# Performance work log

Hardware: AMD Instinct MI355X
Metric: run time of the kernel (lower is better)

The kernel has to match this reference:

```python
import jax, jax.numpy as jnp
import numpy as np
from jax import lax

# Static model/config sizes
B, ANG, C, H, NF, NB = 1, 9, 3, 128, 16, 2


def get_freq_position(n):
    """Anti-diagonal frequency bands of an n x n angular-DCT grid (python/static)."""
    bands = []
    for i in range(n):
        bands.append(([i], [0]))
    for j in range(1, n):
        bands.append(([n - 1], [j]))
    for item in bands:
        while item[0][0] > 0 and item[1][0] < n - 1:
            item[0].insert(0, item[0][0] - 1)
            item[1].insert(0, item[1][0] + 1)
    return bands


def dct_mat(n):
    """Orthonormal DCT-II matrix (row k = k-th basis)."""
    k = jnp.arange(n, dtype=jnp.float32)[:, None]
    i = jnp.arange(n, dtype=jnp.float32)[None, :]
    m = jnp.cos(jnp.pi * (i + 0.5) * k / n) * jnp.sqrt(2.0 / n)
    return m.at[0].multiply(1.0 / np.sqrt(2.0))


def conv3d(x, w, b):
    # x: (N, Cin, D, H, W), w: (Cout, Cin, 3, 3, 3)
    y = lax.conv_general_dilated(x, w, (1, 1, 1), 'SAME',
                                 dimension_numbers=('NCDHW', 'OIDHW', 'NCDHW'))
    return y + b[None, :, None, None, None]


def branch(cut, wi, bi, a, wb, bb):
    """init conv + NB ResBlock3D (PReLU -> Conv3d, residual), plus outer skip."""
    y0 = conv3d(cut, wi, bi)
    y = y0
    for k in range(NB):
        r = jnp.where(y >= 0, y, a[k] * y)  # PReLU (single-parameter)
        y = y + conv3d(r, wb[k], bb[k])
    return y0 + y


def setup_inputs() -> dict:
    key = jax.random.key(0)
    ks = jax.random.split(key, 32)

    def nrm(k, shape, s=0.05):
        return jax.random.normal(k, shape, dtype=jnp.float32) * s

    inp = {"x": jax.random.normal(ks[0], (B, ANG, ANG, C, H, H), dtype=jnp.float32)}
    i = 1
    for n in ("dc", "lo", "mi", "hi"):
        inp[f"w_{n}_i"] = nrm(ks[i], (NF, C, 3, 3, 3)); i += 1
        inp[f"b_{n}_i"] = nrm(ks[i], (NF,)); i += 1
        inp[f"a_{n}"] = jnp.full((NB,), 0.25, dtype=jnp.float32)
        inp[f"w_{n}"] = nrm(ks[i], (NB, NF, NF, 3, 3, 3)); i += 1
        inp[f"b_{n}"] = nrm(ks[i], (NB, NF)); i += 1
    inp["w_last"] = nrm(ks[i], (C, NF))  # 1x1 Conv2d, no bias
    return inp


def reference(x, w_dc_i, b_dc_i, a_dc, w_dc, b_dc,
              w_lo_i, b_lo_i, a_lo, w_lo, b_lo,
              w_mi_i, b_mi_i, a_mi, w_mi, b_mi,
              w_hi_i, b_hi_i, a_hi, w_hi, b_hi, w_last):
    b, u, v, c, h, w = x.shape
    Da = dct_mat(u)  # angular DCT (u == v)
    Ds = dct_mat(h)  # spatial DCT (h == w)

    # SpaAngDCT: spatial 2D DCT then angular 2D DCT
    xf = jnp.einsum('buvchw,Hh,Ww->buvcHW', x, Ds, Ds)
    xf = jnp.einsum('buvchw,Uu,Vv->bUVchw', xf, Da, Da)

    x_rec = jnp.zeros((b, NF, u, v, h, w), dtype=x.dtype)
    for idx, (ui, vi) in enumerate(get_freq_position(u)):
        if idx == 0:
            p = (w_dc_i, b_dc_i, a_dc, w_dc, b_dc)
        elif idx <= 2:
            p = (w_lo_i, b_lo_i, a_lo, w_lo, b_lo)
        elif idx <= u - 1:
            p = (w_mi_i, b_mi_i, a_mi, w_mi, b_mi)
        else:
            p = (w_hi_i, b_hi_i, a_hi, w_hi, b_hi)
        ua, va = jnp.array(ui), jnp.array(vi)
        cut = xf[:, ua, va].transpose(0, 2, 1, 3, 4)  # (b, c, L, h, w)
        out = branch(cut, *p)                          # (b, NF, L, h, w)
        x_rec = x_rec.at[:, :, ua, va].set(out)        # scatter band back

    # 'b c u v h w -> b c (u h) (v w)' then 1x1 conv (NF -> 3)
    xr = x_rec.transpose(0, 1, 2, 4, 3, 5).reshape(b, NF, u * h, v * w)
    xr = jnp.einsum('bnHW,on->boHW', xr, w_last)
    xr = xr.reshape(b, c, u, h, v, w).transpose(0, 2, 4, 1, 3, 5)  # (b,u,v,c,h,w)

    # InverseSpaAngDCT: angular IDCT then spatial IDCT
    xr = jnp.einsum('bUVchw,Uu,Vv->buvchw', xr, Da, Da)
    xr = jnp.einsum('buvcHW,Hh,Ww->buvchw', xr, Ds, Ds)
    return xr + x
```

## Files before the change

### kernel.cpp

```cpp
#include <hip/hip_runtime.h>
#include <hip/hip_bf16.h>
#include <math.h>

typedef __hip_bfloat16 bf16;
typedef __attribute__((ext_vector_type(8))) short short8;
typedef __attribute__((ext_vector_type(4))) float floatx4;
typedef __attribute__((ext_vector_type(4))) unsigned int uint4v;
typedef __attribute__((ext_vector_type(2))) unsigned int uint2v;

#define HW 16384
#define NSLICE 243

__constant__ int c_s_of_p[81] = {
  0, 1,1, 2,2,2, 3,3,3,3, 4,4,4,4,4, 5,5,5,5,5,5, 6,6,6,6,6,6,6,
  7,7,7,7,7,7,7,7, 8,8,8,8,8,8,8,8,8, 9,9,9,9,9,9,9,9,
  10,10,10,10,10,10,10, 11,11,11,11,11,11, 12,12,12,12,12,
  13,13,13,13, 14,14,14, 15,15, 16};
__constant__ int c_l_of_p[81] = {
  0, 0,1, 0,1,2, 0,1,2,3, 0,1,2,3,4, 0,1,2,3,4,5, 0,1,2,3,4,5,6,
  0,1,2,3,4,5,6,7, 0,1,2,3,4,5,6,7,8, 0,1,2,3,4,5,6,7,
  0,1,2,3,4,5,6, 0,1,2,3,4,5, 0,1,2,3,4, 0,1,2,3, 0,1,2, 0,1, 0};
__constant__ int c_L_of_s[17] = {1,2,3,4,5,6,7,8,9,8,7,6,5,4,3,2,1};
__constant__ int c_g_of_s[17] = {0,1,1,2,2,2,2,2,2,3,3,3,3,3,3,3,3};
__constant__ int c_pos_uv[81] = {
  0,1,3,6,10,15,21,28,36,
  2,4,7,11,16,22,29,37,45,
  5,8,12,17,23,30,38,46,53,
  9,13,18,24,31,39,47,54,60,
  14,19,25,32,40,48,55,61,66,
  20,26,33,41,49,56,62,67,71,
  27,34,42,50,57,63,68,72,75,
  35,43,51,58,64,69,73,76,78,
  44,52,59,65,70,74,77,79,80};

struct WPtrs {
  const float* wi[4]; const float* bi[4]; const float* a[4];
  const float* wb[4]; const float* bb[4]; const float* wl;
};

__device__ __forceinline__ unsigned short f2bf(float f) {
  return __bfloat16_as_ushort(__float2bfloat16(f));
}
__device__ __forceinline__ float bflo(unsigned int w) {
  return __uint_as_float(w << 16);
}
__device__ __forceinline__ float bfhi(unsigned int w) {
  return __uint_as_float(w & 0xffff0000u);
}
__device__ __forceinline__ unsigned int pack2(float a, float b) {
  return (unsigned int)f2bf(a) | ((unsigned int)f2bf(b) << 16);
}
__device__ __forceinline__ float invprelu(float v, float invA) {
  return (v >= 0.f) ? v : v * invA;
}
__device__ __forceinline__ void bfsplit(float v, unsigned short& hi, unsigned short& lo) {
  unsigned int bits = __float_as_uint(v);
  hi = (unsigned short)(bits >> 16);
  lo = f2bf(v - __uint_as_float(bits & 0xffff0000u));
}

__global__ __launch_bounds__(256) void k_setup(float* DaF,
                                               unsigned short* TFhi, unsigned short* TFlo,
                                               unsigned short* TIhi, unsigned short* TIlo) {
  const double PI = 3.14159265358979323846;
  int t = blockIdx.x * 256 + threadIdx.x;
  if (t < 81) {
    int U = t / 9, u = t % 9;
    double d = cos(PI * (u + 0.5) * U / 9.0) * sqrt(2.0 / 9.0);
    if (U == 0) d *= (1.0 / sqrt(2.0));
    DaF[t] = (float)d;
  }
  if (t < 16384) {
    int jj = t & 7, lane = (t >> 3) & 63, ks = (t >> 9) & 3, tile = t >> 11;
    int row = tile * 16 + (lane & 15);
    int colk = ks * 32 + (lane >> 4) * 8 + jj;
    double vF = cos(PI * (colk + 0.5) * row / 128.0) * sqrt(2.0 / 128.0);
    if (row == 0) vF *= (1.0 / sqrt(2.0));
    double vI = cos(PI * (row + 0.5) * colk / 128.0) * sqrt(2.0 / 128.0);
    if (colk == 0) vI *= (1.0 / sqrt(2.0));
    unsigned short h, l;
    bfsplit((float)vF, h, l); TFhi[t] = h; TFlo[t] = l;
    bfsplit((float)vI, h, l); TIhi[t] = h; TIlo[t] = l;
  }
}

__global__ __launch_bounds__(256) void k_prep(WPtrs P, unsigned short* Wmf,
                                              float* BiF, float* BbF,
                                              float* AF, float* WlF) {
  int t = blockIdx.x * 256 + threadIdx.x;
  if (t < 92160) {
    int s = t / 7680, r = t % 7680;
    int step = r / 512, r2 = r % 512;
    int lane = r2 >> 3, j = r2 & 7;
    int d = step / 5, i = step % 5;
    int q = lane >> 4, m = lane & 15;
    int tl = 2 * i + (q >> 1);
    int cin = (q & 1) * 8 + j;
    float val = 0.f;
    if (tl <= 8) {
      int ky = tl / 3, kx = tl % 3;
      int tap = d * 9 + ky * 3 + kx;
      if (s < 4) {
        if (cin < 3) val = P.wi[s][(m * 3 + cin) * 27 + tap];
      } else {
        int g = (s - 4) >> 1, k = (s - 4) & 1;
        val = P.wb[g][((k * 16 + m) * 16 + cin) * 27 + tap];
      }
    }
    Wmf[t] = f2bf(val);
  }
  if (t < 64)  BiF[t] = P.bi[t / 16][t % 16];
  if (t < 128) BbF[t] = P.bb[t / 32][t % 32];
  if (t < 8)   AF[t]  = P.a[t / 2][t % 2];
  if (t < 48)  WlF[t] = P.wl[t];
}

__global__ __launch_bounds__(256) void k_dct2(const float* __restrict__ X,
                                              const unsigned short* __restrict__ tabhi,
                                              const unsigned short* __restrict__ tablo,
                                              const float* __restrict__ xres,
                                              float* __restrict__ Y) {
  __shared__ unsigned short sThi[128 * 136];
  __shared__ unsigned short sTlo[128 * 136];
  int s = blockIdx.x;
  int t = threadIdx.x;
  int lane = t & 63, wv = t >> 6;
  int q = lane >> 4, n16 = lane & 15;
  const float* Xs = X + (size_t)s * HW;

  floatx4 acc[2][8];
#pragma unroll
  for (int mt = 0; mt < 2; mt++)
#pragma unroll
    for (int nt = 0; nt < 8; nt++) acc[mt][nt] = (floatx4){0.f, 0.f, 0.f, 0.f};

#pragma unroll
  for (int ks = 0; ks < 4; ks++) {
    short8 ahi[2], alo[2];
#pragma unroll
    for (int mt = 0; mt < 2; mt++) {
      const float* xp = Xs + (wv * 32 + mt * 16 + n16) * 128 + ks * 32 + q * 8;
      float4 a = *(const float4*)xp;
      float4 b = *(const float4*)(xp + 4);
      union { short8 v; unsigned short u[8]; } H, L;
      float xv[8] = {a.x, a.y, a.z, a.w, b.x, b.y, b.z, b.w};
#pragma unroll
      for (int j = 0; j < 8; j++) bfsplit(xv[j], H.u[j], L.u[j]);
      ahi[mt] = H.v; alo[mt] = L.v;
    }
#pragma unroll
    for (int nt = 0; nt < 8; nt++) {
      int e = nt * 2048 + ks * 512 + lane * 8;
      short8 bh = *(const short8*)(tabhi + e);
      short8 bl = *(const short8*)(tablo + e);
#pragma unroll
      for (int mt = 0; mt < 2; mt++) {
        acc[mt][nt] = __builtin_amdgcn_mfma_f32_16x16x32_bf16(ahi[mt], bl, acc[mt][nt], 0, 0, 0);
        acc[mt][nt] = __builtin_amdgcn_mfma_f32_16x16x32_bf16(alo[mt], bh, acc[mt][nt], 0, 0, 0);
        acc[mt][nt] = __builtin_amdgcn_mfma_f32_16x16x32_bf16(ahi[mt], bh, acc[mt][nt], 0, 0, 0);
      }
    }
  }

#pragma unroll
  for (int mt = 0; mt < 2; mt++)
#pragma unroll
    for (int nt = 0; nt < 8; nt++) {
      int col = nt * 16 + n16;
      int rowb = wv * 32 + mt * 16 + q * 4;
#pragma unroll
      for (int rp = 0; rp < 4; rp += 2) {
        unsigned short h0, l0, h1, l1;
        bfsplit(acc[mt][nt][rp], h0, l0);
        bfsplit(acc[mt][nt][rp + 1], h1, l1);
        int widx = (col * 136 + rowb + rp) >> 1;
        ((unsigned int*)sThi)[widx] = (unsigned int)h0 | ((unsigned int)h1 << 16);
        ((unsigned int*)sTlo)[widx] = (unsigned int)l0 | ((unsigned int)l1 << 16);
      }
    }
  __syncthreads();

#pragma unroll
  for (int mt = 0; mt < 2; mt++)
#pragma unroll
    for (int nt = 0; nt < 8; nt++) acc[mt][nt] = (floatx4){0.f, 0.f, 0.f, 0.f};

#pragma unroll
  for (int ks = 0; ks < 4; ks++) {
    short8 ahi[2], alo[2];
#pragma unroll
    for (int mt = 0; mt < 2; mt++) {
      int e = (wv * 2 + mt) * 2048 + ks * 512 + lane * 8;
      ahi[mt] = *(const short8*)(tabhi + e);
      alo[mt] = *(const short8*)(tablo + e);
    }
#pragma unroll
    for (int nt = 0; nt < 8; nt++) {
      int off = (nt * 16 + n16) * 136 + ks * 32 + q * 8;
      short8 bh = *(const short8*)(sThi + off);
      short8 bl = *(const short8*)(sTlo + off);
#pragma unroll
      for (int mt = 0; mt < 2; mt++) {
        acc[mt][nt] = __builtin_amdgcn_mfma_f32_16x16x32_bf16(ahi[mt], bl, acc[mt][nt], 0, 0, 0);
        acc[mt][nt] = __builtin_amdgcn_mfma_f32_16x16x32_bf16(alo[mt], bh, acc[mt][nt], 0, 0, 0);
        acc[mt][nt] = __builtin_amdgcn_mfma_f32_16x16x32_bf16(ahi[mt], bh, acc[mt][nt], 0, 0, 0);
      }
    }
  }

#pragma unroll
  for (int mt = 0; mt < 2; mt++)
#pragma unroll
    for (int nt = 0; nt < 8; nt++) {
      int row0 = wv * 32 + mt * 16 + q * 4;
      int col = nt * 16 + n16;
#pragma unroll
      for (int r = 0; r < 4; r++) {
        size_t oi = (size_t)s * HW + (size_t)(row0 + r) * 128 + col;
        float v = acc[mt][nt][r];
        if (xres) v += xres[oi];
        Y[oi] = v;
      }
    }
}

__global__ __launch_bounds__(256) void k_angu(const float* __restrict__ in,
                                              const float* __restrict__ DaF,
                                              float* __restrict__ out) {
  __shared__ float sDa[81];
  int t = threadIdx.x;
  if (t < 81) sDa[t] = DaF[t];
  __syncthreads();
  int idx = blockIdx.x * 256 + t;
  int hw = idx & (HW - 1);
  int r = idx >> 14;
  int c = r % 3, v = r / 3;
  float f[9];
#pragma unroll
  for (int u = 0; u < 9; u++) f[u] = in[(size_t)((u * 9 + v) * 3 + c) * HW + hw];
#pragma unroll
  for (int U = 0; U < 9; U++) {
    float acc = 0.f;
#pragma unroll
    for (int u = 0; u < 9; u++) acc += sDa[U * 9 + u] * f[u];
    out[(size_t)((U * 9 + v) * 3 + c) * HW + hw] = acc;
  }
}

__global__ __launch_bounds__(256) void k_angv(const float* __restrict__ in,
                                              const float* __restrict__ DaF,
                                              unsigned short* __restrict__ xf2b) {
  __shared__ float sDa[81];
  int t = threadIdx.x;
  if (t < 81) sDa[t] = DaF[t];
  __syncthreads();
  int idx = blockIdx.x * 256 + t;
  int hw = idx & (HW - 1);
  int r = idx >> 14;
  int c = r % 3, U = r / 3;
  float f[9];
#pragma unroll
  for (int v = 0; v < 9; v++) f[v] = in[(size_t)((U * 9 + v) * 3 + c) * HW + hw];
#pragma unroll
  for (int V = 0; V < 9; V++) {
    float acc = 0.f;
#pragma unroll
    for (int v = 0; v < 9; v++) acc += sDa[V * 9 + v] * f[v];
    size_t base = ((size_t)c_pos_uv[U * 9 + V] * HW + hw) * 4;
    xf2b[base + c] = f2bf(acc);
    if (c == 0) xf2b[base + 3] = 0;
  }
}

__global__ __launch_bounds__(256) void k_angvi(const float* __restrict__ xrb,
                                               const float* __restrict__ DaF,
                                               float* __restrict__ out) {
  __shared__ float sDa[81];
  int t = threadIdx.x;
  if (t < 81) sDa[t] = DaF[t];
  __syncthreads();
  int idx = blockIdx.x * 256 + t;
  int hw = idx & (HW - 1);
  int r = idx >> 14;
  int c = r % 3, U = r / 3;
  float f[9];
#pragma unroll
  for (int V = 0; V < 9; V++)
    f[V] = xrb[((size_t)c_pos_uv[U * 9 + V] * 3 + c) * HW + hw];
#pragma unroll
  for (int v = 0; v < 9; v++) {
    float acc = 0.f;
#pragma unroll
    for (int V = 0; V < 9; V++) acc += sDa[V * 9 + v] * f[V];
    out[(size_t)((U * 9 + v) * 3 + c) * HW + hw] = acc;
  }
}

__global__ __launch_bounds__(256) void k_angui(const float* __restrict__ in,
                                               const float* __restrict__ DaF,
                                               float* __restrict__ out) {
  __shared__ float sDa[81];
  int t = threadIdx.x;
  if (t < 81) sDa[t] = DaF[t];
  __syncthreads();
  int idx = blockIdx.x * 256 + t;
  int hw = idx & (HW - 1);
  int r = idx >> 14;
  int c = r % 3, v = r / 3;
  float f[9];
#pragma unroll
  for (int U = 0; U < 9; U++) f[U] = in[(size_t)((U * 9 + v) * 3 + c) * HW + hw];
#pragma unroll
  for (int u = 0; u < 9; u++) {
    float acc = 0.f;
#pragma unroll
    for (int U = 0; U < 9; U++) acc += sDa[U * 9 + u] * f[U];
    out[(size_t)((u * 9 + v) * 3 + c) * HW + hw] = acc;
  }
}

__global__ __launch_bounds__(512) void k_conv(const unsigned short* __restrict__ src,
                                              const unsigned short* __restrict__ prevAct,
                                              const unsigned short* __restrict__ act0,
                                              const unsigned short* __restrict__ Wmf,
                                              const float* __restrict__ BiF,
                                              const float* __restrict__ BbF,
                                              const float* __restrict__ AF,
                                              const float* __restrict__ WlF,
                                              int sel,
                                              unsigned short* __restrict__ boutAct,
                                              float* __restrict__ xrbOut) {
  __shared__ unsigned short s_lds[10 * 132 * 16];
  int p = blockIdx.y;
  int s = c_s_of_p[p], l = c_l_of_p[p];
  int g = c_g_of_s[s], Ls = c_L_of_s[s];
  int row0 = blockIdx.x * 8;
  int t = threadIdx.x;
  int lane = t & 63, wv = t >> 6;
  int q = lane >> 4, n = lane & 15;

  float aNext = (sel < 2) ? AF[g * 2 + sel] : 0.f;
  float invA  = (sel > 0) ? 1.0f / AF[g * 2 + sel - 1] : 0.f;

  int scol = t & 127;
  int shalf = (t >> 7) & 1;
  int srow0 = t >> 8;

  {
    uint4v z = (uint4v){0u, 0u, 0u, 0u};
    int zmax = (sel == 0) ? 1320 : 40;
    for (int i = t; i < zmax; i += 512) {
      int row, half, col;
      if (i < 40) { row = i >> 2; half = (i >> 1) & 1; col = (i & 1) ? 129 : 0; }
      else { int j = i - 40; row = j >> 7; col = (j & 127) + 1; half = 1; }
      *(uint4v*)((char*)s_lds + (size_t)(((row * 2 + half) * 132 + col)) * 16) = z;
    }
  }

  int basel = wv * 4224 + (q & 1) * 2112 + n * 16;
  int off2[5];
#pragma unroll
  for (int i = 0; i < 5; i++) {
    int tl = 2 * i + (q >> 1);
    if (tl > 8) tl = 8;
    int ky = tl / 3, kx = tl % 3;
    off2[i] = basel + ky * 4224 + kx * 16;
  }

  int setIdx = (sel == 0) ? g : (4 + g * 2 + (sel - 1));
  const char* WsetBase = (const char*)Wmf + (size_t)setIdx * 15 * 1024;

  floatx4 acc[8];
#pragma unroll
  for (int cg = 0; cg < 8; cg++) acc[cg] = (floatx4){0.f, 0.f, 0.f, 0.f};

  for (int d = 0; d < 3; d++) {
    int l2 = l + d - 1;
    if (l2 < 0 || l2 >= Ls) continue;
    int p2 = p + d - 1;
    __syncthreads();
    if (sel == 0) {
      if (shalf == 0) {
#pragma unroll
        for (int it = 0; it < 5; it++) {
          int row = srow0 + it * 2;
          int grow = row0 - 1 + row;
          uint2v v2 = (uint2v){0u, 0u};
          if ((unsigned)grow < 128u)
            v2 = *(const uint2v*)(src + ((size_t)p2 * HW + grow * 128 + scol) * 4);
          uint4v val; val.x = v2.x; val.y = v2.y; val.z = 0u; val.w = 0u;
          *(uint4v*)((char*)s_lds + (size_t)((row * 2) * 132 + scol + 1) * 16) = val;
        }
      }
    } else {
#pragma unroll
      for (int it = 0; it < 5; it++) {
        int row = srow0 + it * 2;
        int grow = row0 - 1 + row;
        uint4v val = (uint4v){0u, 0u, 0u, 0u};
        if ((unsigned)grow < 128u)
          val = *(const uint4v*)(src +
              (((size_t)p2 * HW + grow * 128 + scol) * 16 + shalf * 8));
        *(uint4v*)((char*)s_lds + (size_t)((row * 2 + shalf) * 132 + scol + 1) * 16) = val;
      }
    }
    __syncthreads();
    short8 af[5];
#pragma unroll
    for (int i = 0; i < 5; i++)
      af[i] = *(const short8*)(WsetBase + ((d * 5 + i) * 64 + lane) * 16);
#pragma unroll
    for (int cg = 0; cg < 8; cg++) {
#pragma unroll
      for (int i = 0; i < 5; i++) {
        short8 b = *(const short8*)((const char*)s_lds + off2[i] + cg * 256);
        acc[cg] = __builtin_amdgcn_mfma_f32_16x16x32_bf16(af[i], b, acc[cg], 0, 0, 0);
      }
    }
  }

  const float* bp = (sel == 0) ? (BiF + g * 16) : (BbF + g * 32 + (sel - 1) * 16);
  float bz[4];
#pragma unroll
  for (int r = 0; r < 4; r++) bz[r] = bp[q * 4 + r];
  int h = row0 + wv;

  if (sel < 2) {
#pragma unroll
    for (int cg = 0; cg < 8; cg++) {
      size_t pix = (size_t)p * HW + h * 128 + cg * 16 + n;
      float r0 = acc[cg][0] + bz[0], r1 = acc[cg][1] + bz[1];
      float r2 = acc[cg][2] + bz[2], r3 = acc[cg][3] + bz[3];
      if (sel != 0) {
        uint2v pv = *(const uint2v*)(prevAct + pix * 16 + q * 4);
        r0 += invprelu(bflo(pv.x), invA); r1 += invprelu(bfhi(pv.x), invA);
        r2 += invprelu(bflo(pv.y), invA); r3 += invprelu(bfhi(pv.y), invA);
      }
      r0 = fmaxf(r0, 0.f) + aNext * fminf(r0, 0.f);
      r1 = fmaxf(r1, 0.f) + aNext * fminf(r1, 0.f);
      r2 = fmaxf(r2, 0.f) + aNext * fminf(r2, 0.f);
      r3 = fmaxf(r3, 0.f) + aNext * fminf(r3, 0.f);
      uint2v ov; ov.x = pack2(r0, r1); ov.y = pack2(r2, r3);
      *(uint2v*)(boutAct + pix * 16 + q * 4) = ov;
    }
  } else {
    float invA0 = 1.0f / AF[g * 2];
    float wl0[4], wl1[4], wl2[4];
#pragma unroll
    for (int r = 0; r < 4; r++) {
      wl0[r] = WlF[q * 4 + r];
      wl1[r] = WlF[16 + q * 4 + r];
      wl2[r] = WlF[32 + q * 4 + r];
    }
#pragma unroll
    for (int cg = 0; cg < 8; cg++) {
      size_t pix = (size_t)p * HW + h * 128 + cg * 16 + n;
      float r0 = acc[cg][0] + bz[0], r1 = acc[cg][1] + bz[1];
      float r2 = acc[cg][2] + bz[2], r3 = acc[cg][3] + bz[3];
      uint2v pv = *(const uint2v*)(prevAct + pix * 16 + q * 4);
      r0 += invprelu(bflo(pv.x), invA); r1 += invprelu(bfhi(pv.x), invA);
      r2 += invprelu(bflo(pv.y), invA); r3 += invprelu(bfhi(pv.y), invA);
      uint2v p0 = *(const uint2v*)(act0 + pix * 16 + q * 4);
      r0 += invprelu(bflo(p0.x), invA0); r1 += invprelu(bfhi(p0.x), invA0);
      r2 += invprelu(bflo(p0.y), invA0); r3 += invprelu(bfhi(p0.y), invA0);
      float o0 = wl0[0] * r0 + wl0[1] * r1 + wl0[2] * r2 + wl0[3] * r3;
      float o1 = wl1[0] * r0 + wl1[1] * r1 + wl1[2] * r2 + wl1[3] * r3;
      float o2 = wl2[0] * r0 + wl2[1] * r1 + wl2[2] * r2 + wl2[3] * r3;
      o0 += __shfl_xor(o0, 16); o0 += __shfl_xor(o0, 32);
      o1 += __shfl_xor(o1, 16); o1 += __shfl_xor(o1, 32);
      o2 += __shfl_xor(o2, 16); o2 += __shfl_xor(o2, 32);
      if (q == 0) {
        size_t hw = (size_t)h * 128 + cg * 16 + n;
        xrbOut[((size_t)p * 3 + 0) * HW + hw] = o0;
        xrbOut[((size_t)p * 3 + 1) * HW + hw] = o1;
        xrbOut[((size_t)p * 3 + 2) * HW + hw] = o2;
      }
    }
  }
}

extern "C" void kernel_launch(void* const* d_in, const int* in_sizes, int n_in,
                              void* d_out, int out_size, void* d_ws, size_t ws_size,
                              hipStream_t stream) {
  (void)in_sizes; (void)n_in; (void)out_size; (void)ws_size;
  const float* x = (const float*)d_in[0];
  WPtrs P;
  for (int g = 0; g < 4; g++) {
    int b = 1 + g * 5;
    P.wi[g] = (const float*)d_in[b + 0];
    P.bi[g] = (const float*)d_in[b + 1];
    P.a[g]  = (const float*)d_in[b + 2];
    P.wb[g] = (const float*)d_in[b + 3];
    P.bb[g] = (const float*)d_in[b + 4];
  }
  P.wl = (const float*)d_in[21];

  char* base = (char*)d_ws;
  size_t off = 0;
  auto take = [&](size_t bytes) -> char* {
    char* r = base + off;
    off += (bytes + 255) & ~(size_t)255;
    return r;
  };
  float* DaF = (float*)take(81 * 4);
  unsigned short* TFhi = (unsigned short*)take(16384 * 2);
  unsigned short* TFlo = (unsigned short*)take(16384 * 2);
  unsigned short* TIhi = (unsigned short*)take(16384 * 2);
  unsigned short* TIlo = (unsigned short*)take(16384 * 2);
  unsigned short* Wmf = (unsigned short*)take(92160 * 2);
  float* BiF   = (float*)take(256);
  float* BbF   = (float*)take(512);
  float* AF    = (float*)take(32);
  float* WlF   = (float*)take(192);
  float* R1 = (float*)take((size_t)NSLICE * HW * 4);
  float* R2 = (float*)take((size_t)NSLICE * HW * 4);
  float* R3 = (float*)take((size_t)NSLICE * HW * 4);
  unsigned short* braw0 = (unsigned short*)take((size_t)81 * 16 * HW * 2);
  unsigned short* braw1 = (unsigned short*)take((size_t)81 * 16 * HW * 2);
  unsigned short* xf2b = (unsigned short*)R3;
  float* xrb = R3;

  k_setup<<<64, 256, 0, stream>>>(DaF, TFhi, TFlo, TIhi, TIlo);
  k_prep<<<360, 256, 0, stream>>>(P, Wmf, BiF, BbF, AF, WlF);
  k_dct2<<<243, 256, 0, stream>>>(x, TFhi, TFlo, nullptr, R1);
  k_angu<<<1728, 256, 0, stream>>>(R1, DaF, R2);
  k_angv<<<1728, 256, 0, stream>>>(R2, DaF, xf2b);
  k_conv<<<dim3(16, 81), 512, 0, stream>>>(xf2b, nullptr, nullptr, Wmf,
                                           BiF, BbF, AF, WlF, 0, braw0, nullptr);
  k_conv<<<dim3(16, 81), 512, 0, stream>>>(braw0, braw0, nullptr, Wmf,
                                           BiF, BbF, AF, WlF, 1, braw1, nullptr);
  k_conv<<<dim3(16, 81), 512, 0, stream>>>(braw1, braw1, braw0, Wmf,
                                           BiF, BbF, AF, WlF, 2, nullptr, xrb);
  k_angvi<<<1728, 256, 0, stream>>>(xrb, DaF, R2);
  k_angui<<<1728, 256, 0, stream>>>(R2, DaF, R1);
  k_dct2<<<243, 256, 0, stream>>>(R1, TIhi, TIlo, x, (float*)d_out);
}
```

Baseline: 299.3 us.

## Fuse angular DCT passes via LDS and use direct global-to-LDS loads in conv

Merges the two forward angular DCT passes (u then v) into one kernel that stages all 81 angular samples per pixel in LDS, and does the same for the two inverse passes. This removes an intermediate full-size fp32 buffer round trip through global memory. Separately, the conv kernel's activation staging now uses global_load_lds to copy straight into shared memory, and zero-fills out-of-range halo rows once up front instead of every tap. The fused angular kernels launch only 384 small blocks, each using about 41 KB of LDS, which may leave the GPU underoccupied.

Result: no change. 301.7 us (+0.8%).

```diff
diff --git a/kernel.cpp b/kernel.cpp
--- a/kernel.cpp
+++ b/kernel.cpp
@@ -58,6 +58,11 @@
   hi = (unsigned short)(bits >> 16);
   lo = f2bf(v - __uint_as_float(bits & 0xffff0000u));
 }
+__device__ __forceinline__ void gl_lds16(const void* g, void* l) {
+  __builtin_amdgcn_global_load_lds(
+      (const __attribute__((address_space(1))) unsigned int*)g,
+      (__attribute__((address_space(3))) unsigned int*)l, 16, 0, 0);
+}
 
 __global__ __launch_bounds__(256) void k_setup(float* DaF,
                                                unsigned short* TFhi, unsigned short* TFlo,
@@ -224,98 +229,83 @@
     }
 }
 
-__global__ __launch_bounds__(256) void k_angu(const float* __restrict__ in,
+__global__ __launch_bounds__(128) void k_angF(const float* __restrict__ xf1,
                                               const float* __restrict__ DaF,
-                                              float* __restrict__ out) {
+                                              unsigned short* __restrict__ xf2b) {
+  __shared__ float L[81 * 128];
   __shared__ float sDa[81];
   int t = threadIdx.x;
+  int c = blockIdx.y;
+  int hw = blockIdx.x * 128 + t;
   if (t < 81) sDa[t] = DaF[t];
   __syncthreads();
-  int idx = blockIdx.x * 256 + t;
-  int hw = idx & (HW - 1);
-  int r = idx >> 14;
-  int c = r % 3, v = r / 3;
-  float f[9];
-#pragma unroll
-  for (int u = 0; u < 9; u++) f[u] = in[(size_t)((u * 9 + v) * 3 + c) * HW + hw];
-#pragma unroll
+#pragma unroll 3
+  for (int i = 0; i < 81; i++)
+    L[i * 128 + t] = xf1[(size_t)(i * 3 + c) * HW + hw];
+  for (int v = 0; v < 9; v++) {
+    float f[9];
+#pragma unroll
+    for (int u = 0; u < 9; u++) f[u] = L[(u * 9 + v) * 128 + t];
+#pragma unroll
+    for (int U = 0; U < 9; U++) {
+      float a = 0.f;
+#pragma unroll
+      for (int u = 0; u < 9; u++) a += sDa[U * 9 + u] * f[u];
+      L[(U * 9 + v) * 128 + t] = a;
+    }
+  }
   for (int U = 0; U < 9; U++) {
-    float acc = 0.f;
-#pragma unroll
-    for (int u = 0; u < 9; u++) acc += sDa[U * 9 + u] * f[u];
-    out[(size_t)((U * 9 + v) * 3 + c) * HW + hw] = acc;
-  }
-}
-
-__global__ __launch_bounds__(256) void k_angv(const float* __restrict__ in,
+    float f[9];
+#pragma unroll
+    for (int v = 0; v < 9; v++) f[v] = L[(U * 9 + v) * 128 + t];
+#pragma unroll
+    for (int V = 0; V < 9; V++) {
+      float a = 0.f;
+#pragma unroll
+      for (int v = 0; v < 9; v++) a += sDa[V * 9 + v] * f[v];
+      size_t base = ((size_t)c_pos_uv[U * 9 + V] * HW + hw) * 4;
+      xf2b[base + c] = f2bf(a);
+      if (c == 0) xf2b[base + 3] = 0;
+    }
+  }
+}
+
+__global__ __launch_bounds__(128) void k_angI(const float* __restrict__ xrb,
                                               const float* __restrict__ DaF,
-                                              unsigned short* __restrict__ xf2b) {
+                                              float* __restrict__ xr2) {
+  __shared__ float L[81 * 128];
   __shared__ float sDa[81];
   int t = threadIdx.x;
+  int c = blockIdx.y;
+  int hw = blockIdx.x * 128 + t;
   if (t < 81) sDa[t] = DaF[t];
   __syncthreads();
-  int idx = blockIdx.x * 256 + t;
-  int hw = idx & (HW - 1);
-  int r = idx >> 14;
-  int c = r % 3, U = r / 3;
-  float f[9];
-#pragma unroll
-  for (int v = 0; v < 9; v++) f[v] = in[(size_t)((U * 9 + v) * 3 + c) * HW + hw];
-#pragma unroll
-  for (int V = 0; V < 9; V++) {
-    float acc = 0.f;
-#pragma unroll
-    for (int v = 0; v < 9; v++) acc += sDa[V * 9 + v] * f[v];
-    size_t base = ((size_t)c_pos_uv[U * 9 + V] * HW + hw) * 4;
-    xf2b[base + c] = f2bf(acc);
-    if (c == 0) xf2b[base + 3] = 0;
-  }
-}
-
-__global__ __launch_bounds__(256) void k_angvi(const float* __restrict__ xrb,
-                                               const float* __restrict__ DaF,
-                                               float* __restrict__ out) {
-  __shared__ float sDa[81];
-  int t = threadIdx.x;
-  if (t < 81) sDa[t] = DaF[t];
-  __syncthreads();
-  int idx = blockIdx.x * 256 + t;
-  int hw = idx & (HW - 1);
-  int r = idx >> 14;
-  int c = r % 3, U = r / 3;
-  float f[9];
-#pragma unroll
-  for (int V = 0; V < 9; V++)
-    f[V] = xrb[((size_t)c_pos_uv[U * 9 + V] * 3 + c) * HW + hw];
-#pragma unroll
+#pragma unroll 3
+  for (int i = 0; i < 81; i++)
+    L[i * 128 + t] = xrb[((size_t)c_pos_uv[i] * 3 + c) * HW + hw];
+  for (int U = 0; U < 9; U++) {
+    float f[9];
+#pragma unroll
+    for (int V = 0; V < 9; V++) f[V] = L[(U * 9 + V) * 128 + t];
+#pragma unroll
+    for (int v = 0; v < 9; v++) {
+      float a = 0.f;
+#pragma unroll
+      for (int V = 0; V < 9; V++) a += sDa[V * 9 + v] * f[V];
+      L[(U * 9 + v) * 128 + t] = a;
+    }
+  }
   for (int v = 0; v < 9; v++) {
-    float acc = 0.f;
-#pragma unroll
-    for (int V = 0; V < 9; V++) acc += sDa[V * 9 + v] * f[V];
-    out[(size_t)((U * 9 + v) * 3 + c) * HW + hw] = acc;
-  }
-}
-
-__global__ __launch_bounds__(256) void k_angui(const float* __restrict__ in,
-                                               const float* __restrict__ DaF,
-                                               float* __restrict__ out) {
-  __shared__ float sDa[81];
-  int t = threadIdx.x;
-  if (t < 81) sDa[t] = DaF[t];
-  __syncthreads();
-  int idx = blockIdx.x * 256 + t;
-  int hw = idx & (HW - 1);
-  int r = idx >> 14;
-  int c = r % 3, v = r / 3;
-  float f[9];
-#pragma unroll
-  for (int U = 0; U < 9; U++) f[U] = in[(size_t)((U * 9 + v) * 3 + c) * HW + hw];
-#pragma unroll
-  for (int u = 0; u < 9; u++) {
-    float acc = 0.f;
-#pragma unroll
-    for (int U = 0; U < 9; U++) acc += sDa[U * 9 + u] * f[U];
-    out[(size_t)((u * 9 + v) * 3 + c) * HW + hw] = acc;
+    float f[9];
+#pragma unroll
+    for (int U = 0; U < 9; U++) f[U] = L[(U * 9 + v) * 128 + t];
+#pragma unroll
+    for (int u = 0; u < 9; u++) {
+      float a = 0.f;
+#pragma unroll
+      for (int U = 0; U < 9; U++) a += sDa[U * 9 + u] * f[U];
+      xr2[(size_t)((u * 9 + v) * 3 + c) * HW + hw] = a;
+    }
   }
 }
 
@@ -355,6 +345,15 @@
       else { int j = i - 40; row = j >> 7; col = (j & 127) + 1; half = 1; }
       *(uint4v*)((char*)s_lds + (size_t)(((row * 2 + half) * 132 + col)) * 16) = z;
     }
+    for (int row = 0; row < 10; row++) {
+      int grow = row0 - 1 + row;
+      if ((unsigned)grow >= 128u) {
+        for (int i = t; i < 264; i += 512) {
+          int half = i / 132, col = i % 132;
+          *(uint4v*)((char*)s_lds + (size_t)((row * 2 + half) * 132 + col) * 16) = z;
+        }
+      }
+    }
   }
 
   int basel = wv * 4224 + (q & 1) * 2112 + n * 16;
@@ -385,11 +384,11 @@
         for (int it = 0; it < 5; it++) {
           int row = srow0 + it * 2;
           int grow = row0 - 1 + row;
-          uint2v v2 = (uint2v){0u, 0u};
-          if ((unsigned)grow < 128u)
-            v2 = *(const uint2v*)(src + ((size_t)p2 * HW + grow * 128 + scol) * 4);
-          uint4v val; val.x = v2.x; val.y = v2.y; val.z = 0u; val.w = 0u;
-          *(uint4v*)((char*)s_lds + (size_t)((row * 2) * 132 + scol + 1) * 16) = val;
+          if ((unsigned)grow < 128u) {
+            uint2v v2 = *(const uint2v*)(src + ((size_t)p2 * HW + grow * 128 + scol) * 4);
+            uint4v val; val.x = v2.x; val.y = v2.y; val.z = 0u; val.w = 0u;
+            *(uint4v*)((char*)s_lds + (size_t)((row * 2) * 132 + scol + 1) * 16) = val;
+          }
         }
       }
     } else {
@@ -397,11 +396,13 @@
       for (int it = 0; it < 5; it++) {
         int row = srow0 + it * 2;
         int grow = row0 - 1 + row;
-        uint4v val = (uint4v){0u, 0u, 0u, 0u};
-        if ((unsigned)grow < 128u)
-          val = *(const uint4v*)(src +
-              (((size_t)p2 * HW + grow * 128 + scol) * 16 + shalf * 8));
-        *(uint4v*)((char*)s_lds + (size_t)((row * 2 + shalf) * 132 + scol + 1) * 16) = val;
+        if ((unsigned)grow < 128u) {
+          const void* gp = (const void*)(src +
+              (((size_t)p2 * HW + (size_t)grow * 128 + scol) * 16 + shalf * 8));
+          void* lp = (void*)((char*)s_lds +
+              (size_t)((row * 2 + shalf) * 132 + (wv & 1) * 64 + 1) * 16);
+          gl_lds16(gp, lp);
+        }
       }
     }
     __syncthreads();
@@ -513,7 +514,6 @@
   float* AF    = (float*)take(32);
   float* WlF   = (float*)take(192);
   float* R1 = (float*)take((size_t)NSLICE * HW * 4);
-  float* R2 = (float*)take((size_t)NSLICE * HW * 4);
   float* R3 = (float*)take((size_t)NSLICE * HW * 4);
   unsigned short* braw0 = (unsigned short*)take((size_t)81 * 16 * HW * 2);
   unsigned short* braw1 = (unsigned short*)take((size_t)81 * 16 * HW * 2);
@@ -523,15 +523,13 @@
   k_setup<<<64, 256, 0, stream>>>(DaF, TFhi, TFlo, TIhi, TIlo);
   k_prep<<<360, 256, 0, stream>>>(P, Wmf, BiF, BbF, AF, WlF);
   k_dct2<<<243, 256, 0, stream>>>(x, TFhi, TFlo, nullptr, R1);
-  k_angu<<<1728, 256, 0, stream>>>(R1, DaF, R2);
-  k_angv<<<1728, 256, 0, stream>>>(R2, DaF, xf2b);
+  k_angF<<<dim3(128, 3), 128, 0, stream>>>(R1, DaF, xf2b);
   k_conv<<<dim3(16, 81), 512, 0, stream>>>(xf2b, nullptr, nullptr, Wmf,
                                            BiF, BbF, AF, WlF, 0, braw0, nullptr);
   k_conv<<<dim3(16, 81), 512, 0, stream>>>(braw0, braw0, nullptr, Wmf,
                                            BiF, BbF, AF, WlF, 1, braw1, nullptr);
   k_conv<<<dim3(16, 81), 512, 0, stream>>>(braw1, braw1, braw0, Wmf,
                                            BiF, BbF, AF, WlF, 2, nullptr, xrb);
-  k_angvi<<<1728, 256, 0, stream>>>(xrb, DaF, R2);
-  k_angui<<<1728, 256, 0, stream>>>(R2, DaF, R1);
+  k_angI<<<dim3(128, 3), 128, 0, stream>>>(xrb, DaF, R1);
   k_dct2<<<243, 256, 0, stream>>>(R1, TIhi, TIlo, x, (float*)d_out);
 }
```
